# Optimization experiments

Hardware: AMD Instinct MI355X
Metric: run time of the kernel (lower is better)

The kernel has to match this reference:

```python
import jax, jax.numpy as jnp
import numpy as np

G, N, E, C = 4, 50000, 800000, 128


def setup_inputs() -> dict:
    key = jax.random.key(0)
    ks = jax.random.split(key, 8)
    x = jax.random.normal(ks[0], (G, N, C), dtype=jnp.float32)
    edge_index = jax.random.randint(ks[1], (G, 2, E), 0, N, dtype=jnp.int64)
    s = 1.0 / np.sqrt(C)
    W1 = jax.random.normal(ks[2], (G, C, C), dtype=jnp.float32) * s
    W2 = jax.random.normal(ks[3], (G, C, C), dtype=jnp.float32) * s
    W3 = jax.random.normal(ks[4], (G, C, C), dtype=jnp.float32) * s
    b1 = jnp.zeros((G, C), dtype=jnp.float32)
    b2 = jnp.zeros((G, C), dtype=jnp.float32)
    b3 = jnp.zeros((G, C), dtype=jnp.float32)
    return {"x": x, "edge_index": edge_index, "W1": W1, "b1": b1,
            "W2": W2, "b2": b2, "W3": W3, "b3": b3}


def _gcn_layer(x, src, dst, deg_inv_sqrt, W, b):
    # PyG GCNConv: linear, then D^-1/2 (A+I) D^-1/2 aggregation, then bias.
    h = x @ W                                   # [N, C_out]
    norm = deg_inv_sqrt[src] * deg_inv_sqrt[dst]  # [E+N]
    msg = h[src] * norm[:, None]                # gather + scale
    out = jax.ops.segment_sum(msg, dst, num_segments=x.shape[0])
    return out + b


def _forward_one(x, ei, W1, b1, W2, b2, W3, b3):
    n = x.shape[0]
    loops = jnp.arange(n, dtype=ei.dtype)
    src = jnp.concatenate([ei[0], loops])       # add self-loops
    dst = jnp.concatenate([ei[1], loops])
    deg = jax.ops.segment_sum(jnp.ones_like(src, dtype=x.dtype), dst, num_segments=n)
    dis = jnp.where(deg > 0, jax.lax.rsqrt(deg), 0.0)
    x = _gcn_layer(x, src, dst, dis, W1, b1)
    x = _gcn_layer(x, src, dst, dis, W2, b2)
    x = _gcn_layer(x, src, dst, dis, W3, b3)
    return x


def reference(x, edge_index, W1, b1, W2, b2, W3, b3):
    # vmap over the num_graphs independent GCN stacks, then concat node dim
    out = jax.vmap(_forward_one)(x, edge_index, W1, b1, W2, b2, W3, b3)
    return out.reshape(-1, out.shape[-1])       # [G*N, out_channels]
```

## Files before the change

### kernel.cpp

```cpp
#include <hip/hip_runtime.h>

#define NG 4
#define NN 50000
#define NE 800000
#define NC 128
#define NB 196
#define NBT (NG * NB)
#define CAPB 48
#define LBS (NB + 1)
#define CAPQ 4608
#define GEMM_BLKS 784

typedef _Float16 half8 __attribute__((ext_vector_type(8)));
typedef _Float16 half4 __attribute__((ext_vector_type(4)));
typedef float f32x4 __attribute__((ext_vector_type(4)));

__global__ __launch_bounds__(256) void init_cursors(int* __restrict__ bktCur) {
  int i = blockIdx.x * blockDim.x + threadIdx.x;
  if (i < NBT) bktCur[i] = i * CAPQ;
}

__global__ __launch_bounds__(512) void fat_gemm1_scatter(
    const float* __restrict__ x, const float* __restrict__ W,
    _Float16* __restrict__ h, const int* __restrict__ ei,
    int* __restrict__ bktCur, unsigned int* __restrict__ rec) {
  __shared__ char smem[65536];
  int bid = blockIdx.x;
  int tid = threadIdx.x;
  if (bid < GEMM_BLKS) {
    _Float16* Wt0 = (_Float16*)smem;
    _Float16* Wt1 = Wt0 + 128 * 128;
    int g = bid / 196;
    int row0 = (bid % 196) * 256;
    int lane = tid & 63;
    int wv = tid >> 6;
    int kc = lane >> 4;
    int lr = lane & 15;
    const float* Wg = W + (size_t)g * NC * NC;
    const float* xg = x + (size_t)g * NN * NC;
    {
      int n = tid & 127;
      int kq = (tid >> 7) & 3;
      #pragma unroll
      for (int it = 0; it < 8; ++it) {
        int k4 = it * 16 + kq * 4;
        float w0 = Wg[(size_t)(k4 + 0) * NC + n];
        float w1 = Wg[(size_t)(k4 + 1) * NC + n];
        float w2 = Wg[(size_t)(k4 + 2) * NC + n];
        float w3 = Wg[(size_t)(k4 + 3) * NC + n];
        half4 hi, lo;
        hi[0] = (_Float16)w0; lo[0] = (_Float16)(w0 - (float)hi[0]);
        hi[1] = (_Float16)w1; lo[1] = (_Float16)(w1 - (float)hi[1]);
        hi[2] = (_Float16)w2; lo[2] = (_Float16)(w2 - (float)hi[2]);
        hi[3] = (_Float16)w3; lo[3] = (_Float16)(w3 - (float)hi[3]);
        int chunk = k4 >> 3;
        int base = n * 128 + ((chunk ^ (n & 15)) << 3) + (k4 & 4);
        *(half4*)&Wt0[base] = hi;
        *(half4*)&Wt1[base] = lo;
      }
    }
    __syncthreads();
    f32x4 acc[2][8];
    #pragma unroll
    for (int mb = 0; mb < 2; ++mb)
      #pragma unroll
      for (int nb = 0; nb < 8; ++nb)
        acc[mb][nb] = (f32x4){0.f, 0.f, 0.f, 0.f};
    for (int kstep = 0; kstep < 4; ++kstep) {
      half8 ah[2], al[2];
      #pragma unroll
      for (int mb = 0; mb < 2; ++mb) {
        int row = row0 + wv * 32 + mb * 16 + lr;
        if (row > NN - 1) row = NN - 1;
        const float* xp = xg + (size_t)row * NC + kstep * 32 + kc * 8;
        float4 v0 = *(const float4*)xp;
        float4 v1 = *(const float4*)(xp + 4);
        float vv[8] = {v0.x, v0.y, v0.z, v0.w, v1.x, v1.y, v1.z, v1.w};
        #pragma unroll
        for (int i = 0; i < 8; ++i) {
          _Float16 t = (_Float16)vv[i];
          ah[mb][i] = t; al[mb][i] = (_Float16)(vv[i] - (float)t);
        }
      }
      #pragma unroll
      for (int nb = 0; nb < 8; ++nb) {
        int n = nb * 16 + lr;
        int chunk = kstep * 4 + kc;
        int boff = n * 128 + ((chunk ^ (n & 15)) << 3);
        half8 bh = *(const half8*)&Wt0[boff];
        half8 bl = *(const half8*)&Wt1[boff];
        #pragma unroll
        for (int mb = 0; mb < 2; ++mb) {
          acc[mb][nb] = __builtin_amdgcn_mfma_f32_16x16x32_f16(ah[mb], bh, acc[mb][nb], 0, 0, 0);
          acc[mb][nb] = __builtin_amdgcn_mfma_f32_16x16x32_f16(al[mb], bh, acc[mb][nb], 0, 0, 0);
          acc[mb][nb] = __builtin_amdgcn_mfma_f32_16x16x32_f16(ah[mb], bl, acc[mb][nb], 0, 0, 0);
        }
      }
    }
    _Float16* hg = h + (size_t)g * NN * NC;
    #pragma unroll
    for (int mb = 0; mb < 2; ++mb) {
      #pragma unroll
      for (int reg = 0; reg < 4; ++reg) {
        int row = row0 + wv * 32 + mb * 16 + kc * 4 + reg;
        if (row < NN) {
          half8 o;
          #pragma unroll
          for (int nb = 0; nb < 8; ++nb)
            o[nb] = (_Float16)acc[mb][nb][reg];
          *(half8*)(hg + (size_t)row * NC + lr * 8) = o;
        }
      }
    }
  } else {
    int* lcnt = (int*)smem;
    int* lbase = lcnt + NB;
    unsigned int* lbin = (unsigned int*)(smem + 2048);
    int sb = bid - GEMM_BLKS;
    int g = sb / 196;
    int e0 = (sb % 196) * 4096;
    for (int i = tid; i < NB; i += 512) lcnt[i] = 0;
    __syncthreads();
    const int* srcp = ei + (size_t)g * 2 * NE;
    const int* dstp = srcp + NE;
    for (int t = tid; t < 4096; t += 512) {
      int e = e0 + t;
      if (e < NE) {
        int s = srcp[e], d = dstp[e];
        int b = d >> 8;
        unsigned int r = ((unsigned int)(d & 255) << 16) | (unsigned int)s;
        int pos = atomicAdd(&lcnt[b], 1);
        if (pos < CAPB) lbin[pos * LBS + b] = r;
        else { int gp = atomicAdd(&bktCur[g * NB + b], 1); rec[gp] = r; }
      }
    }
    __syncthreads();
    if (tid < NB) {
      int n = lcnt[tid]; if (n > CAPB) n = CAPB;
      lbase[tid] = n ? atomicAdd(&bktCur[g * NB + tid], n) : 0;
    }
    __syncthreads();
    int lane = tid & 63, wv = tid >> 6;
    for (int b = wv; b < NB; b += 8) {
      int n = lcnt[b]; if (n > CAPB) n = CAPB;
      if (lane < n) rec[lbase[b] + lane] = lbin[lane * LBS + b];
    }
  }
}

__global__ __launch_bounds__(256) void build_csr(
    const unsigned int* __restrict__ rec, const int* __restrict__ bktCur,
    unsigned short* __restrict__ col, int* __restrict__ off,
    unsigned short* __restrict__ deg, float* __restrict__ dis) {
  __shared__ int cnt[256];
  __shared__ int offv[256];
  __shared__ int cnt2[256];
  __shared__ int wsum[4];
  int g = blockIdx.y, b = blockIdx.x;
  int idx = g * NB + b;
  int rb = idx * CAPQ, re = bktCur[idx];
  int tid = threadIdx.x;
  cnt[tid] = 0;
  __syncthreads();
  for (int j = rb + tid; j < re; j += 256)
    atomicAdd(&cnt[(rec[j] >> 16) & 255], 1);
  __syncthreads();
  int lane = tid & 63, wv = tid >> 6;
  int v = cnt[tid], incl = v;
  #pragma unroll
  for (int d2 = 1; d2 < 64; d2 <<= 1) {
    int t = __shfl_up(incl, d2, 64);
    if (lane >= d2) incl += t;
  }
  if (lane == 63) wsum[wv] = incl;
  __syncthreads();
  if (tid == 0) {
    int s = 0;
    #pragma unroll
    for (int w = 0; w < 4; ++w) { int t = wsum[w]; wsum[w] = s; s += t; }
  }
  __syncthreads();
  int excl = wsum[wv] + incl - v;
  offv[tid] = excl;
  cnt2[tid] = 0;
  int node = b * 256 + tid;
  if (node < NN) {
    off[g * (NN + 1) + node] = rb + excl;
    deg[(size_t)g * NN + node] = (unsigned short)v;
    dis[(size_t)g * NN + node] = rsqrtf((float)(v + 1));
  }
  __syncthreads();
  for (int j = rb + tid; j < re; j += 256) {
    unsigned int r = rec[j];
    int dl = (r >> 16) & 255;
    int p = rb + offv[dl] + atomicAdd(&cnt2[dl], 1);
    col[p] = (unsigned short)(r & 0xFFFF);
  }
}

__global__ __launch_bounds__(512) void gemm16_mfma_kernel(
    const _Float16* __restrict__ x, const float* __restrict__ W,
    const float* __restrict__ dis, _Float16* __restrict__ h) {
  __shared__ _Float16 Wt[2][128 * 128];
  int g = blockIdx.y;
  int row0 = blockIdx.x * 256;
  int tid = threadIdx.x;
  int lane = tid & 63;
  int wv = tid >> 6;
  int kc = lane >> 4;
  int lr = lane & 15;
  const float* Wg = W + (size_t)g * NC * NC;
  const _Float16* xg = x + (size_t)g * NN * NC;
  {
    int n = tid & 127;
    int kq = (tid >> 7) & 3;
    #pragma unroll
    for (int it = 0; it < 8; ++it) {
      int k4 = it * 16 + kq * 4;
      float w0 = Wg[(size_t)(k4 + 0) * NC + n];
      float w1 = Wg[(size_t)(k4 + 1) * NC + n];
      float w2 = Wg[(size_t)(k4 + 2) * NC + n];
      float w3 = Wg[(size_t)(k4 + 3) * NC + n];
      half4 hi, lo;
      hi[0] = (_Float16)w0; lo[0] = (_Float16)(w0 - (float)hi[0]);
      hi[1] = (_Float16)w1; lo[1] = (_Float16)(w1 - (float)hi[1]);
      hi[2] = (_Float16)w2; lo[2] = (_Float16)(w2 - (float)hi[2]);
      hi[3] = (_Float16)w3; lo[3] = (_Float16)(w3 - (float)hi[3]);
      int chunk = k4 >> 3;
      int base = n * 128 + ((chunk ^ (n & 15)) << 3) + (k4 & 4);
      *(half4*)&Wt[0][base] = hi;
      *(half4*)&Wt[1][base] = lo;
    }
  }
  __syncthreads();
  f32x4 acc[2][8];
  #pragma unroll
  for (int mb = 0; mb < 2; ++mb)
    #pragma unroll
    for (int nb = 0; nb < 8; ++nb)
      acc[mb][nb] = (f32x4){0.f, 0.f, 0.f, 0.f};
  for (int kstep = 0; kstep < 4; ++kstep) {
    half8 ah[2];
    #pragma unroll
    for (int mb = 0; mb < 2; ++mb) {
      int row = row0 + wv * 32 + mb * 16 + lr;
      if (row > NN - 1) row = NN - 1;
      ah[mb] = *(const half8*)(xg + (size_t)row * NC + kstep * 32 + kc * 8);
    }
    #pragma unroll
    for (int nb = 0; nb < 8; ++nb) {
      int n = nb * 16 + lr;
      int chunk = kstep * 4 + kc;
      int boff = n * 128 + ((chunk ^ (n & 15)) << 3);
      half8 bh = *(const half8*)&Wt[0][boff];
      half8 bl = *(const half8*)&Wt[1][boff];
      #pragma unroll
      for (int mb = 0; mb < 2; ++mb) {
        acc[mb][nb] = __builtin_amdgcn_mfma_f32_16x16x32_f16(ah[mb], bh, acc[mb][nb], 0, 0, 0);
        acc[mb][nb] = __builtin_amdgcn_mfma_f32_16x16x32_f16(ah[mb], bl, acc[mb][nb], 0, 0, 0);
      }
    }
  }
  const float* disg = dis + (size_t)g * NN;
  _Float16* hg = h + (size_t)g * NN * NC;
  #pragma unroll
  for (int mb = 0; mb < 2; ++mb) {
    #pragma unroll
    for (int reg = 0; reg < 4; ++reg) {
      int row = row0 + wv * 32 + mb * 16 + kc * 4 + reg;
      if (row < NN) {
        float dsc = disg[row];
        half8 o;
        #pragma unroll
        for (int nb = 0; nb < 8; ++nb)
          o[nb] = (_Float16)(acc[mb][nb][reg] * dsc);
        *(half8*)(hg + (size_t)row * NC + lr * 8) = o;
      }
    }
  }
}

#define MIXACC(A, H) A = fmaf((float)(H), 1.0f, A)
#define MIXS(A, H, S) A = fmaf((float)(H), S, A)
template <bool F16OUT, bool GDIS>
__global__ __launch_bounds__(256) void agg_kernel(
    const _Float16* __restrict__ h, const int* __restrict__ off,
    const unsigned short* __restrict__ col, const unsigned short* __restrict__ deg,
    const float* __restrict__ dis, const float* __restrict__ b,
    float* __restrict__ outf, _Float16* __restrict__ outh) {
  int bid = blockIdx.x;
  int g = (bid & 7) >> 1;
  int sub = ((bid >> 3) << 1) | (bid & 1);
  int node = sub * 16 + (threadIdx.x >> 4);
  if (sub >= NN / 16) return;
  int l = threadIdx.x & 15;
  const half8* h8 = (const half8*)(h + (size_t)g * NN * NC);
  const float* disg = dis + (size_t)g * NN;
  float dn = disg[node];
  float a0[8], a1[8], a2[8], a3[8];
  half8 v = h8[(size_t)node * 16 + l];
  #pragma unroll
  for (int i = 0; i < 8; ++i) {
    a0[i] = GDIS ? dn * (float)v[i] : (float)v[i];
    a1[i] = 0.f; a2[i] = 0.f; a3[i] = 0.f;
  }
  int s = off[g * (NN + 1) + node];
  int e = s + deg[(size_t)g * NN + node];
  int j = s;
  for (; j + 4 <= e; j += 4) {
    int c0 = col[j], c1 = col[j + 1], c2 = col[j + 2], c3 = col[j + 3];
    half8 v0 = h8[(size_t)c0 * 16 + l];
    half8 v1 = h8[(size_t)c1 * 16 + l];
    half8 v2 = h8[(size_t)c2 * 16 + l];
    half8 v3 = h8[(size_t)c3 * 16 + l];
    if constexpr (GDIS) {
      float d0 = disg[c0], d1 = disg[c1], d2 = disg[c2], d3 = disg[c3];
      #pragma unroll
      for (int i = 0; i < 8; ++i) {
        MIXS(a0[i], v0[i], d0); MIXS(a1[i], v1[i], d1);
        MIXS(a2[i], v2[i], d2); MIXS(a3[i], v3[i], d3);
      }
    } else {
      #pragma unroll
      for (int i = 0; i < 8; ++i) {
        MIXACC(a0[i], v0[i]); MIXACC(a1[i], v1[i]);
        MIXACC(a2[i], v2[i]); MIXACC(a3[i], v3[i]);
      }
    }
  }
  for (; j < e; ++j) {
    int c = col[j];
    half8 vr = h8[(size_t)c * 16 + l];
    if constexpr (GDIS) {
      float dd = disg[c];
      #pragma unroll
      for (int i = 0; i < 8; ++i) MIXS(a0[i], vr[i], dd);
    } else {
      #pragma unroll
      for (int i = 0; i < 8; ++i) MIXACC(a0[i], vr[i]);
    }
  }
  const float* bg = b + (size_t)g * NC;
  if constexpr (F16OUT) {
    _Float16* og = outh + ((size_t)g * NN + node) * NC;
    #pragma unroll
    for (int i = 0; i < 8; ++i) {
      float val = (a0[i] + a1[i] + a2[i] + a3[i]) * dn + bg[i * 16 + l];
      og[i * 16 + l] = (_Float16)val;
    }
  } else {
    float* og = outf + ((size_t)g * NN + node) * NC;
    #pragma unroll
    for (int i = 0; i < 8; ++i) {
      float val = (a0[i] + a1[i] + a2[i] + a3[i]) * dn + bg[i * 16 + l];
      og[i * 16 + l] = val;
    }
  }
}

extern "C" void kernel_launch(void* const* d_in, const int* in_sizes, int n_in,
                              void* d_out, int out_size, void* d_ws, size_t ws_size,
                              hipStream_t stream) {
  const float* x  = (const float*)d_in[0];
  const int*   ei = (const int*)d_in[1];
  const float* W1 = (const float*)d_in[2];
  const float* b1 = (const float*)d_in[3];
  const float* W2 = (const float*)d_in[4];
  const float* b2 = (const float*)d_in[5];
  const float* W3 = (const float*)d_in[6];
  const float* b3 = (const float*)d_in[7];
  float* out = (float*)d_out;

  char* ws = (char*)d_ws;
  size_t p = 0;
  auto carve = [&](size_t bytes) -> char* {
    char* r = ws + p;
    p += (bytes + 255) & ~(size_t)255;
    return r;
  };
  int*            bktCur = (int*)           carve((size_t)NBT * 4);
  unsigned short* col    = (unsigned short*)carve((size_t)NBT * CAPQ * 2);
  int*            off    = (int*)           carve((size_t)NG * (NN + 1) * 4);
  unsigned short* deg    = (unsigned short*)carve((size_t)NG * NN * 2);
  float*          dis    = (float*)         carve((size_t)NG * NN * 4);
  _Float16*       hbuf   = (_Float16*)      carve((size_t)NG * NN * NC * 2);
  size_t ubytes = (size_t)NG * NN * NC * 2;
  char*           uni    = carve(ubytes);
  unsigned int*   rec    = (unsigned int*)uni;
  _Float16*       xh     = (_Float16*)uni;

  init_cursors<<<(NBT + 255) / 256, 256, 0, stream>>>(bktCur);
  fat_gemm1_scatter<<<GEMM_BLKS + 784, 512, 0, stream>>>(x, W1, hbuf, ei, bktCur, rec);
  build_csr<<<dim3(NB, NG), 256, 0, stream>>>(rec, bktCur, col, off, deg, dis);

  dim3 ggrid((NN + 255) / 256, NG);
  int  agrid = ((NN / 16 + 1) / 2) * 8;

  agg_kernel<true, true><<<agrid, 256, 0, stream>>>(hbuf, off, col, deg, dis, b1, nullptr, xh);
  gemm16_mfma_kernel<<<ggrid, 512, 0, stream>>>(xh, W2, dis, hbuf);
  agg_kernel<true, false><<<agrid, 256, 0, stream>>>(hbuf, off, col, deg, dis, b2, nullptr, xh);
  gemm16_mfma_kernel<<<ggrid, 512, 0, stream>>>(xh, W3, dis, hbuf);
  agg_kernel<false, false><<<agrid, 256, 0, stream>>>(hbuf, off, col, deg, dis, b3, out, nullptr);
}
```

Baseline: 443.4 us.

## Split feature columns across XCD halves in intermediate aggregation with permuted slot layout

Result: slower. 461.7 us (+4.1%).

```diff
diff --git a/kernel.cpp b/kernel.cpp
--- a/kernel.cpp
+++ b/kernel.cpp
@@ -217,10 +217,14 @@
     #pragma unroll
     for (int it = 0; it < 8; ++it) {
       int k4 = it * 16 + kq * 4;
-      float w0 = Wg[(size_t)(k4 + 0) * NC + n];
-      float w1 = Wg[(size_t)(k4 + 1) * NC + n];
-      float w2 = Wg[(size_t)(k4 + 2) * NC + n];
-      float w3 = Wg[(size_t)(k4 + 3) * NC + n];
+      int t0 = (((k4 + 0) & 7) << 4) | ((k4 + 0) >> 3);
+      int t1 = (((k4 + 1) & 7) << 4) | ((k4 + 1) >> 3);
+      int t2 = (((k4 + 2) & 7) << 4) | ((k4 + 2) >> 3);
+      int t3 = (((k4 + 3) & 7) << 4) | ((k4 + 3) >> 3);
+      float w0 = Wg[(size_t)t0 * NC + n];
+      float w1 = Wg[(size_t)t1 * NC + n];
+      float w2 = Wg[(size_t)t2 * NC + n];
+      float w3 = Wg[(size_t)t3 * NC + n];
       half4 hi, lo;
       hi[0] = (_Float16)w0; lo[0] = (_Float16)(w0 - (float)hi[0]);
       hi[1] = (_Float16)w1; lo[1] = (_Float16)(w1 - (float)hi[1]);
@@ -282,12 +286,86 @@
 
 #define MIXACC(A, H) A = fmaf((float)(H), 1.0f, A)
 #define MIXS(A, H, S) A = fmaf((float)(H), S, A)
-template <bool F16OUT, bool GDIS>
-__global__ __launch_bounds__(256) void agg_kernel(
+template <bool GDIS>
+__global__ __launch_bounds__(256) void agg_slot_kernel(
     const _Float16* __restrict__ h, const int* __restrict__ off,
     const unsigned short* __restrict__ col, const unsigned short* __restrict__ deg,
     const float* __restrict__ dis, const float* __restrict__ b,
-    float* __restrict__ outf, _Float16* __restrict__ outh) {
+    _Float16* __restrict__ outh) {
+  int bid = blockIdx.x;
+  int xcd = bid & 7;
+  int g = xcd >> 1;
+  int hh = xcd & 1;
+  int sub = bid >> 3;
+  int node = sub * 16 + (threadIdx.x >> 4);
+  if (node >= NN) return;
+  int l = threadIdx.x & 15;
+  int so = hh * 64 + l * 4;
+  const _Float16* hp = h + (size_t)g * NN * NC + so;
+  const float* disg = dis + (size_t)g * NN;
+  float dn = disg[node];
+  float bv[4];
+  #pragma unroll
+  for (int i = 0; i < 4; ++i) {
+    int p = so + i;
+    bv[i] = b[(size_t)g * NC + (((p & 7) << 4) | (p >> 3))];
+  }
+  float a0[4], a1[4], a2[4], a3[4];
+  half4 v = *(const half4*)(hp + (size_t)node * NC);
+  #pragma unroll
+  for (int i = 0; i < 4; ++i) {
+    a0[i] = GDIS ? dn * (float)v[i] : (float)v[i];
+    a1[i] = 0.f; a2[i] = 0.f; a3[i] = 0.f;
+  }
+  int s = off[g * (NN + 1) + node];
+  int e = s + deg[(size_t)g * NN + node];
+  int j = s;
+  for (; j + 4 <= e; j += 4) {
+    int c0 = col[j], c1 = col[j + 1], c2 = col[j + 2], c3 = col[j + 3];
+    half4 v0 = *(const half4*)(hp + (size_t)c0 * NC);
+    half4 v1 = *(const half4*)(hp + (size_t)c1 * NC);
+    half4 v2 = *(const half4*)(hp + (size_t)c2 * NC);
+    half4 v3 = *(const half4*)(hp + (size_t)c3 * NC);
+    if constexpr (GDIS) {
+      float d0 = disg[c0], d1 = disg[c1], d2 = disg[c2], d3 = disg[c3];
+      #pragma unroll
+      for (int i = 0; i < 4; ++i) {
+        MIXS(a0[i], v0[i], d0); MIXS(a1[i], v1[i], d1);
+        MIXS(a2[i], v2[i], d2); MIXS(a3[i], v3[i], d3);
+      }
+    } else {
+      #pragma unroll
+      for (int i = 0; i < 4; ++i) {
+        MIXACC(a0[i], v0[i]); MIXACC(a1[i], v1[i]);
+        MIXACC(a2[i], v2[i]); MIXACC(a3[i], v3[i]);
+      }
+    }
+  }
+  for (; j < e; ++j) {
+    int c = col[j];
+    half4 vr = *(const half4*)(hp + (size_t)c * NC);
+    if constexpr (GDIS) {
+      float dd = disg[c];
+      #pragma unroll
+      for (int i = 0; i < 4; ++i) MIXS(a0[i], vr[i], dd);
+    } else {
+      #pragma unroll
+      for (int i = 0; i < 4; ++i) MIXACC(a0[i], vr[i]);
+    }
+  }
+  _Float16* og = outh + ((size_t)g * NN + node) * NC + so;
+  half4 o;
+  #pragma unroll
+  for (int i = 0; i < 4; ++i)
+    o[i] = (_Float16)((a0[i] + a1[i] + a2[i] + a3[i]) * dn + bv[i]);
+  *(half4*)og = o;
+}
+
+__global__ __launch_bounds__(256) void agg_final_kernel(
+    const _Float16* __restrict__ h, const int* __restrict__ off,
+    const unsigned short* __restrict__ col, const unsigned short* __restrict__ deg,
+    const float* __restrict__ dis, const float* __restrict__ b,
+    float* __restrict__ outf) {
   int bid = blockIdx.x;
   int g = (bid & 7) >> 1;
   int sub = ((bid >> 3) << 1) | (bid & 1);
@@ -301,8 +379,7 @@
   half8 v = h8[(size_t)node * 16 + l];
   #pragma unroll
   for (int i = 0; i < 8; ++i) {
-    a0[i] = GDIS ? dn * (float)v[i] : (float)v[i];
-    a1[i] = 0.f; a2[i] = 0.f; a3[i] = 0.f;
+    a0[i] = (float)v[i]; a1[i] = 0.f; a2[i] = 0.f; a3[i] = 0.f;
   }
   int s = off[g * (NN + 1) + node];
   int e = s + deg[(size_t)g * NN + node];
@@ -313,48 +390,23 @@
     half8 v1 = h8[(size_t)c1 * 16 + l];
     half8 v2 = h8[(size_t)c2 * 16 + l];
     half8 v3 = h8[(size_t)c3 * 16 + l];
-    if constexpr (GDIS) {
-      float d0 = disg[c0], d1 = disg[c1], d2 = disg[c2], d3 = disg[c3];
-      #pragma unroll
-      for (int i = 0; i < 8; ++i) {
-        MIXS(a0[i], v0[i], d0); MIXS(a1[i], v1[i], d1);
-        MIXS(a2[i], v2[i], d2); MIXS(a3[i], v3[i], d3);
-      }
-    } else {
-      #pragma unroll
-      for (int i = 0; i < 8; ++i) {
-        MIXACC(a0[i], v0[i]); MIXACC(a1[i], v1[i]);
-        MIXACC(a2[i], v2[i]); MIXACC(a3[i], v3[i]);
-      }
+    #pragma unroll
+    for (int i = 0; i < 8; ++i) {
+      MIXACC(a0[i], v0[i]); MIXACC(a1[i], v1[i]);
+      MIXACC(a2[i], v2[i]); MIXACC(a3[i], v3[i]);
     }
   }
   for (; j < e; ++j) {
-    int c = col[j];
-    half8 vr = h8[(size_t)c * 16 + l];
-    if constexpr (GDIS) {
-      float dd = disg[c];
-      #pragma unroll
-      for (int i = 0; i < 8; ++i) MIXS(a0[i], vr[i], dd);
-    } else {
-      #pragma unroll
-      for (int i = 0; i < 8; ++i) MIXACC(a0[i], vr[i]);
-    }
+    half8 vr = h8[(size_t)col[j] * 16 + l];
+    #pragma unroll
+    for (int i = 0; i < 8; ++i) MIXACC(a0[i], vr[i]);
   }
   const float* bg = b + (size_t)g * NC;
-  if constexpr (F16OUT) {
-    _Float16* og = outh + ((size_t)g * NN + node) * NC;
-    #pragma unroll
-    for (int i = 0; i < 8; ++i) {
-      float val = (a0[i] + a1[i] + a2[i] + a3[i]) * dn + bg[i * 16 + l];
-      og[i * 16 + l] = (_Float16)val;
-    }
-  } else {
-    float* og = outf + ((size_t)g * NN + node) * NC;
-    #pragma unroll
-    for (int i = 0; i < 8; ++i) {
-      float val = (a0[i] + a1[i] + a2[i] + a3[i]) * dn + bg[i * 16 + l];
-      og[i * 16 + l] = val;
-    }
+  float* og = outf + ((size_t)g * NN + node) * NC;
+  #pragma unroll
+  for (int i = 0; i < 8; ++i) {
+    float val = (a0[i] + a1[i] + a2[i] + a3[i]) * dn + bg[i * 16 + l];
+    og[i * 16 + l] = val;
   }
 }
 
@@ -394,11 +446,12 @@
   build_csr<<<dim3(NB, NG), 256, 0, stream>>>(rec, bktCur, col, off, deg, dis);
 
   dim3 ggrid((NN + 255) / 256, NG);
-  int  agrid = ((NN / 16 + 1) / 2) * 8;
-
-  agg_kernel<true, true><<<agrid, 256, 0, stream>>>(hbuf, off, col, deg, dis, b1, nullptr, xh);
+  int  agridS = (NN / 16) * 8;
+  int  agridF = ((NN / 16 + 1) / 2) * 8;
+
+  agg_slot_kernel<true><<<agridS, 256, 0, stream>>>(hbuf, off, col, deg, dis, b1, xh);
   gemm16_mfma_kernel<<<ggrid, 512, 0, stream>>>(xh, W2, dis, hbuf);
-  agg_kernel<true, false><<<agrid, 256, 0, stream>>>(hbuf, off, col, deg, dis, b2, nullptr, xh);
+  agg_slot_kernel<false><<<agridS, 256, 0, stream>>>(hbuf, off, col, deg, dis, b2, xh);
   gemm16_mfma_kernel<<<ggrid, 512, 0, stream>>>(xh, W3, dis, hbuf);
-  agg_kernel<false, false><<<agrid, 256, 0, stream>>>(hbuf, off, col, deg, dis, b3, out, nullptr);
-}
+  agg_final_kernel<<<agridF, 256, 0, stream>>>(hbuf, off, col, deg, dis, b3, out);
+}
```
